# Kernel optimization log

Measured on AMD Instinct MI355X. Metric: run time of the kernel, lower is better.

## Reference

```python
import jax, jax.numpy as jnp
import numpy as np

N_FEATURES = 256
N_LAYERS = 256  # MZI layers; 2*N_LAYERS PSBS sublayers
BATCH = 1024


def _make_indexAB(nF):
    A = np.array([[2 * k, 2 * k + 1] for k in range(nF // 2)], np.int32)
    B = [[2 * k + 1, 2 * k + 2] for k in range((nF - 1) // 2)]
    while len(B) < nF // 2:
        B.append([-1, -1])  # padding sentinel, masked out
    return A, np.array(B, np.int32)


def _make_index(nF, nLayers):
    A, B = _make_indexAB(nF)
    blocks = ([A] * 2 + [B] * 2) * (nLayers // 2)
    if nLayers % 2 == 1:
        blocks += [A] * 2
    return np.stack(blocks).astype(np.int32)  # [2*nLayers, nF//2, 2]


def setup_inputs() -> dict:
    key = jax.random.key(0)
    k1, k2, k3 = jax.random.split(key, 3)
    nSub = 2 * N_LAYERS
    nAng = N_FEATURES // 2
    index = jnp.asarray(_make_index(N_FEATURES, N_LAYERS))
    return {
        "x_real": jax.random.normal(k1, (BATCH, N_FEATURES), jnp.float32),
        "x_imag": jax.random.normal(k2, (BATCH, N_FEATURES), jnp.float32),
        "params": jax.random.normal(k3, (nSub, nAng), jnp.float32),  # torch.randn init
        "ps_params": jnp.zeros((N_FEATURES,), jnp.float32),  # ModulePS zeros init
        "index": index,
        "split": jnp.zeros((nSub, nAng), jnp.float32),  # buffer, default zeros
        "atten": jnp.ones((nSub, N_FEATURES), jnp.float32),  # buffer, default ones
    }


def _psbs_mesh(x, params, i_safe, j_safe, valid, split, atten):
    # x: [B, F] complex64. Each sublayer: phase e^{i theta} on top port, then
    # beamsplitter [[cos a, i sin a],[i sin a, cos a]] with a = pi/4 + split,
    # then per-feature diagonal attenuation.
    def step(x, xs):
        theta, isf, jsf, vld, sp, at = xs
        xu = x[:, isf]  # [B, A]
        xv = x[:, jsf]
        u = xu * jnp.exp(1j * theta)[None, :]
        ang = jnp.float32(np.pi / 4) + sp
        t = jnp.cos(ang)
        r = jnp.sin(ang)
        yu = t * u + 1j * r * xv
        yv = 1j * r * u + t * xv
        zero = jnp.zeros((), x.dtype)
        # scatter deltas; invalid (padded) pairs add 0 so duplicate dummy index 0 is safe
        x = x.at[:, isf].add(jnp.where(vld, yu - xu, zero))
        x = x.at[:, jsf].add(jnp.where(vld, yv - xv, zero))
        return x * at[None, :], None

    x, _ = jax.lax.scan(step, x, (params, i_safe, j_safe, valid, split, atten))
    return x


def reference(x_real, x_imag, params, ps_params, index, split, atten):
    x = (x_real + 1j * x_imag).astype(jnp.complex64)
    i_idx = index[:, :, 0]
    j_idx = index[:, :, 1]
    valid = i_idx >= 0
    i_safe = jnp.where(valid, i_idx, 0)
    j_safe = jnp.where(valid, j_idx, 0)
    x = _psbs_mesh(x, params, i_safe, j_safe, valid, split, atten)
    # final diagonal phase shift (ModulePS)
    return x * jnp.exp(1j * ps_params)[None, :]
```

## Files before the change

### kernel.cpp

```cpp
#include <hip/hip_runtime.h>
#include <math.h>

#define NF   256
#define NSUB 512
#define NB   1024
#define BLOBF 768
#define WS_FLOATS (NSUB * BLOBF + NF * 2)
#define PI4 0.78539816339744830962f

__device__ __forceinline__ bool looks_zero(const void* p) {
  const unsigned* u = (const unsigned*)p;
  return (u[1] | u[25] | u[111]) == 0u;
}
__device__ __forceinline__ bool looks_ones(const void* p) {
  const unsigned* u = (const unsigned*)p;
  return u[1] == 0x3F800000u && u[3] == 0x3F800000u && u[257] == 0x3F800000u;
}

__global__ __launch_bounds__(256) void precompute_kernel(
    const void* __restrict__ pp0, const void* __restrict__ pp1,
    const void* __restrict__ pi0, const void* __restrict__ pi1,
    const float* __restrict__ psp, float* __restrict__ ws) {
  const float* params = looks_zero(pp0) ? (const float*)pp1 : (const float*)pp0;
  const float* split  = looks_zero(pp0) ? (const float*)pp0 : (const float*)pp1;
  const float* atten  = looks_ones(pi0) ? (const float*)pi0 : (const float*)pi1;
  const int s = blockIdx.x;
  const int t = threadIdx.x;
  if (s == NSUB) {
    float sn, cs;
    sincosf(psp[t], &sn, &cs);
    ((float2*)(ws + (size_t)NSUB * BLOBF))[t] = make_float2(cs, sn);
    return;
  }
  float* blob = ws + (size_t)s * BLOBF;
  if (t < 128) {
    float sn, cs, rr, tt;
    sincosf(params[s * 128 + t], &sn, &cs);
    sincosf(PI4 + split[s * 128 + t], &rr, &tt);
    *(float4*)(blob + (t >> 1) * 12 + (t & 1) * 4) = make_float4(cs, sn, tt, rr);
  } else if (t < 192) {
    const int l = t - 128;
    *(float4*)(blob + l * 12 + 8) = *(const float4*)(atten + (size_t)s * NF + 4 * l);
  }
}

struct Coef { float4 a, b, c; };

__device__ __forceinline__ Coef loadCoef(const char* p) {
  Coef k;
  k.a = *(const float4*)(p);
  k.b = *(const float4*)(p + 16);
  k.c = *(const float4*)(p + 32);
  return k;
}

__device__ __forceinline__ void mzi(float& ur, float& ui, float& vr, float& vi,
                                    const float4 k) {
  const float c = k.x, s = k.y, t = k.z, r = k.w;
  const float pr  = c * ur - s * ui;
  const float pi_ = s * ur + c * ui;
  const float nur = t * pr  - r * vi;
  const float nui = t * pi_ + r * vr;
  const float nvr = t * vr - r * pi_;
  const float nvi = t * vi + r * pr;
  ur = nur; ui = nui; vr = nvr; vi = nvi;
}

#define STATE float& x0r, float& x0i, float& x1r, float& x1i, \
              float& x2r, float& x2i, float& x3r, float& x3i

__device__ __forceinline__ void layerA(const Coef k, STATE) {
  mzi(x0r, x0i, x1r, x1i, k.a);
  mzi(x2r, x2i, x3r, x3i, k.b);
  x0r *= k.c.x; x0i *= k.c.x; x1r *= k.c.y; x1i *= k.c.y;
  x2r *= k.c.z; x2i *= k.c.z; x3r *= k.c.w; x3i *= k.c.w;
}

__device__ __forceinline__ void layerB(const Coef k, const int lane, STATE) {
  mzi(x1r, x1i, x2r, x2i, k.a);
  const float nvr = __shfl_down(x0r, 1);
  const float nvi = __shfl_down(x0i, 1);
  const float c = k.b.x, s = k.b.y, t = k.b.z, r = k.b.w;
  const float pr  = c * x3r - s * x3i;
  const float pi_ = s * x3r + c * x3i;
  const float yur = t * pr  - r * nvi;
  const float yui = t * pi_ + r * nvr;
  const float yvr = t * nvr - r * pi_;
  const float yvi = t * nvi + r * pr;
  const float svr = __shfl_up(yvr, 1);
  const float svi = __shfl_up(yvi, 1);
  if (lane < 63) { x3r = yur; x3i = yui; }
  if (lane > 0)  { x0r = svr; x0i = svi; }
  x0r *= k.c.x; x0i *= k.c.x; x1r *= k.c.y; x1i *= k.c.y;
  x2r *= k.c.z; x2i *= k.c.z; x3r *= k.c.w; x3i *= k.c.w;
}

__device__ __forceinline__ Coef makeCoefRaw(const float* __restrict__ params,
                                            const float* __restrict__ split,
                                            const float* __restrict__ atten,
                                            int s, int lane) {
  Coef k;
  const float2 th = *(const float2*)(params + (size_t)s * 128 + 2 * lane);
  const float2 sp = *(const float2*)(split + (size_t)s * 128 + 2 * lane);
  k.c = *(const float4*)(atten + (size_t)s * NF + 4 * lane);
  float sn, cs, rr, tt;
  __sincosf(th.x, &sn, &cs);
  __sincosf(PI4 + sp.x, &rr, &tt);
  k.a = make_float4(cs, sn, tt, rr);
  __sincosf(th.y, &sn, &cs);
  __sincosf(PI4 + sp.y, &rr, &tt);
  k.b = make_float4(cs, sn, tt, rr);
  return k;
}

#define PASS x0r, x0i, x1r, x1i, x2r, x2i, x3r, x3i

template <bool USE_WS>
__global__ __launch_bounds__(256) void mesh_kernel(
    const float* __restrict__ xr_in, const float* __restrict__ xi_in,
    const float* __restrict__ ws,
    const void* __restrict__ pp0, const void* __restrict__ pp1,
    const void* __restrict__ pi0, const void* __restrict__ pi1,
    const float* __restrict__ psp,
    float* __restrict__ out) {
  const int lane = threadIdx.x & 63;
  const int wv   = threadIdx.x >> 6;
  const int row  = blockIdx.x * 4 + wv;

  const float4 r4 = ((const float4*)(xr_in + (size_t)row * NF))[lane];
  const float4 i4 = ((const float4*)(xi_in + (size_t)row * NF))[lane];
  float x0r = r4.x, x1r = r4.y, x2r = r4.z, x3r = r4.w;
  float x0i = i4.x, x1i = i4.y, x2i = i4.z, x3i = i4.w;

  if (USE_WS) {
    const char* cp = (const char*)ws + lane * 48;
    Coef k0 = loadCoef(cp);
    Coef k1 = loadCoef(cp + 3072);
    Coef k2 = loadCoef(cp + 2 * 3072);
    Coef k3 = loadCoef(cp + 3 * 3072);
#pragma unroll 1
    for (int s = 0; s < NSUB; s += 4) {
      const char* np = cp + ((s + 4 < NSUB) ? 4 * 3072 : 0);
      Coef n0 = loadCoef(np);
      Coef n1 = loadCoef(np + 3072);
      Coef n2 = loadCoef(np + 2 * 3072);
      Coef n3 = loadCoef(np + 3 * 3072);
      layerA(k0, PASS);
      layerA(k1, PASS);
      layerB(k2, lane, PASS);
      layerB(k3, lane, PASS);
      k0 = n0; k1 = n1; k2 = n2; k3 = n3; cp = np;
    }
  } else {
    const float* params = looks_zero(pp0) ? (const float*)pp1 : (const float*)pp0;
    const float* split  = looks_zero(pp0) ? (const float*)pp0 : (const float*)pp1;
    const float* atten  = looks_ones(pi0) ? (const float*)pi0 : (const float*)pi1;
#pragma unroll 1
    for (int s = 0; s < NSUB; s += 4) {
      Coef k0 = makeCoefRaw(params, split, atten, s, lane);
      layerA(k0, PASS);
      Coef k1 = makeCoefRaw(params, split, atten, s + 1, lane);
      layerA(k1, PASS);
      Coef k2 = makeCoefRaw(params, split, atten, s + 2, lane);
      layerB(k2, lane, PASS);
      Coef k3 = makeCoefRaw(params, split, atten, s + 3, lane);
      layerB(k3, lane, PASS);
    }
  }

  float c0, s0, c1, s1, c2, s2, c3, s3;
  if (USE_WS) {
    const float2* psc = (const float2*)(ws + (size_t)NSUB * BLOBF);
    const float2 p0 = psc[4 * lane + 0];
    const float2 p1 = psc[4 * lane + 1];
    const float2 p2 = psc[4 * lane + 2];
    const float2 p3 = psc[4 * lane + 3];
    c0 = p0.x; s0 = p0.y; c1 = p1.x; s1 = p1.y;
    c2 = p2.x; s2 = p2.y; c3 = p3.x; s3 = p3.y;
  } else {
    sincosf(psp[4 * lane + 0], &s0, &c0);
    sincosf(psp[4 * lane + 1], &s1, &c1);
    sincosf(psp[4 * lane + 2], &s2, &c2);
    sincosf(psp[4 * lane + 3], &s3, &c3);
  }
  const float o0r = x0r * c0 - x0i * s0, o0i = x0r * s0 + x0i * c0;
  const float o1r = x1r * c1 - x1i * s1, o1i = x1r * s1 + x1i * c1;
  const float o2r = x2r * c2 - x2i * s2, o2i = x2r * s2 + x2i * c2;
  const float o3r = x3r * c3 - x3i * s3, o3i = x3r * s3 + x3i * c3;

  float4* op = (float4*)out;
  const size_t base = (size_t)row * 64 + lane;
  op[base] = make_float4(o0r, o1r, o2r, o3r);
  op[(size_t)NB * 64 + base] = make_float4(o0i, o1i, o2i, o3i);
}

extern "C" void kernel_launch(void* const* d_in, const int* in_sizes, int n_in,
                              void* d_out, int out_size, void* d_ws, size_t ws_size,
                              hipStream_t stream) {
  const void* px[2] = { d_in[0], d_in[1] };
  const void* pp[2] = { d_in[2], d_in[5] };
  const void* pi2[2] = { d_in[4], d_in[6] };
  const void* pps = d_in[3];
  {
    const void* sx[2]; const void* sp[2]; const void* si[2];
    const void* s256 = nullptr;
    int nx = 0, npp = 0, ni = 0;
    for (int i = 0; i < n_in; ++i) {
      const int sz = in_sizes[i];
      if (sz == 262144 && nx < 2)      sx[nx++] = d_in[i];
      else if (sz == 65536 && npp < 2) sp[npp++] = d_in[i];
      else if (sz == 131072 && ni < 2) si[ni++] = d_in[i];
      else if (sz == 256)              s256 = d_in[i];
    }
    if (nx == 2)  { px[0] = sx[0];  px[1] = sx[1]; }
    if (npp == 2) { pp[0] = sp[0];  pp[1] = sp[1]; }
    if (ni == 2)  { pi2[0] = si[0]; pi2[1] = si[1]; }
    if (s256)     pps = s256;
  }
  float* out = (float*)d_out;

  const size_t need = (size_t)WS_FLOATS * sizeof(float);
  if (ws_size >= need) {
    float* ws = (float*)d_ws;
    precompute_kernel<<<NSUB + 1, 256, 0, stream>>>(pp[0], pp[1], pi2[0], pi2[1],
                                                    (const float*)pps, ws);
    mesh_kernel<true><<<NB / 4, 256, 0, stream>>>(
        (const float*)px[0], (const float*)px[1], ws,
        pp[0], pp[1], pi2[0], pi2[1], (const float*)pps, out);
  } else {
    mesh_kernel<false><<<NB / 4, 256, 0, stream>>>(
        (const float*)px[0], (const float*)px[1], nullptr,
        pp[0], pp[1], pi2[0], pi2[1], (const float*)pps, out);
  }
}
```

Baseline: 79.90 us.

## Fuse consecutive same-index PSBS sublayer pairs into precomputed 2x2 complex matrices

Consecutive sublayers share the same pairing pattern (AA, BB), so each pair of phase-shift, beamsplitter and attenuation steps is folded into one complex 2x2 matrix per port pair. A precompute kernel writes 256 combined layers, and attenuation on unpaired boundary ports is folded into the matrices and the final phase table. The mesh kernel then does half as many sequential steps, with one shuffle pair per type-B layer, and re-indexes registers to handle the shifted B pairing. The cost is more coefficient data per step (32 vs 24 floats per lane) and more FLOPs per combined step.

```diff
diff --git a/kernel.cpp b/kernel.cpp
--- a/kernel.cpp
+++ b/kernel.cpp
@@ -1,11 +1,12 @@
 #include <hip/hip_runtime.h>
 #include <math.h>
 
-#define NF   256
-#define NSUB 512
-#define NB   1024
-#define BLOBF 768
-#define WS_FLOATS (NSUB * BLOBF + NF * 2)
+#define NF    256
+#define NSUB  512
+#define NB    1024
+#define NCOMB 256
+#define LAYER_F 1024
+#define WS_FLOATS2 (NCOMB * LAYER_F + 2 * NF)
 #define PI4 0.78539816339744830962f
 
 __device__ __forceinline__ bool looks_zero(const void* p) {
@@ -17,41 +18,141 @@
   return u[1] == 0x3F800000u && u[3] == 0x3F800000u && u[257] == 0x3F800000u;
 }
 
-__global__ __launch_bounds__(256) void precompute_kernel(
+__device__ __forceinline__ float2 cmul(float2 a, float2 b) {
+  return make_float2(a.x * b.x - a.y * b.y, a.x * b.y + a.y * b.x);
+}
+__device__ __forceinline__ float2 cadd(float2 a, float2 b) {
+  return make_float2(a.x + b.x, a.y + b.y);
+}
+__device__ __forceinline__ float2 csc(float2 a, float s) {
+  return make_float2(a.x * s, a.y * s);
+}
+
+__global__ __launch_bounds__(128) void precompute2_kernel(
     const void* __restrict__ pp0, const void* __restrict__ pp1,
     const void* __restrict__ pi0, const void* __restrict__ pi1,
     const float* __restrict__ psp, float* __restrict__ ws) {
   const float* params = looks_zero(pp0) ? (const float*)pp1 : (const float*)pp0;
   const float* split  = looks_zero(pp0) ? (const float*)pp0 : (const float*)pp1;
   const float* atten  = looks_ones(pi0) ? (const float*)pi0 : (const float*)pi1;
-  const int s = blockIdx.x;
-  const int t = threadIdx.x;
-  if (s == NSUB) {
-    float sn, cs;
-    sincosf(psp[t], &sn, &cs);
-    ((float2*)(ws + (size_t)NSUB * BLOBF))[t] = make_float2(cs, sn);
+  const int L = blockIdx.x;
+  const int k = threadIdx.x;
+
+  if (L == NCOMB) {
+#pragma unroll
+    for (int h = 0; h < 2; ++h) {
+      const int f = k + h * 128;
+      float sn, cs;
+      sincosf(psp[f], &sn, &cs);
+      if (f == 0) {
+        const float f0s = atten[510 * 256] * atten[511 * 256];
+        cs *= f0s; sn *= f0s;
+      }
+      ((float2*)(ws + (size_t)NCOMB * LAYER_F))[f] = make_float2(cs, sn);
+    }
     return;
   }
-  float* blob = ws + (size_t)s * BLOBF;
-  if (t < 128) {
-    float sn, cs, rr, tt;
-    sincosf(params[s * 128 + t], &sn, &cs);
-    sincosf(PI4 + split[s * 128 + t], &rr, &tt);
-    *(float4*)(blob + (t >> 1) * 12 + (t & 1) * 4) = make_float4(cs, sn, tt, rr);
-  } else if (t < 192) {
-    const int l = t - 128;
-    *(float4*)(blob + l * 12 + 8) = *(const float4*)(atten + (size_t)s * NF + 4 * l);
-  }
-}
-
-struct Coef { float4 a, b, c; };
-
-__device__ __forceinline__ Coef loadCoef(const char* p) {
-  Coef k;
-  k.a = *(const float4*)(p);
-  k.b = *(const float4*)(p + 16);
-  k.c = *(const float4*)(p + 32);
-  return k;
+
+  const int s1 = 2 * L, s2 = s1 + 1;
+  const bool typeB = (L & 1);
+  float2 C00, C01, C10, C11;
+  if (typeB && k == 127) {
+    const float a = atten[(size_t)s1 * NF + 255] * atten[(size_t)s2 * NF + 255];
+    C00 = make_float2(a, 0.f); C01 = make_float2(0.f, 0.f);
+    C10 = make_float2(0.f, 0.f); C11 = make_float2(0.f, 0.f);
+  } else {
+    const int i = typeB ? 2 * k + 1 : 2 * k;
+    const int j = i + 1;
+    float c1, s1v, t1, r1, c2, s2v, t2, r2;
+    sincosf(params[(size_t)s1 * 128 + k], &s1v, &c1);
+    sincosf(PI4 + split[(size_t)s1 * 128 + k], &r1, &t1);
+    sincosf(params[(size_t)s2 * 128 + k], &s2v, &c2);
+    sincosf(PI4 + split[(size_t)s2 * 128 + k], &r2, &t2);
+    const float a1i = atten[(size_t)s1 * NF + i], a1j = atten[(size_t)s1 * NF + j];
+    const float a2i = atten[(size_t)s2 * NF + i], a2j = atten[(size_t)s2 * NF + j];
+    const float2 Q00 = csc(make_float2(t1 * c1, t1 * s1v), a1i);
+    const float2 Q01 = csc(make_float2(0.f, r1), a1i);
+    const float2 Q10 = csc(make_float2(-r1 * s1v, r1 * c1), a1j);
+    const float2 Q11 = csc(make_float2(t1, 0.f), a1j);
+    const float2 P00 = csc(make_float2(t2 * c2, t2 * s2v), a2i);
+    const float2 P01 = csc(make_float2(0.f, r2), a2i);
+    const float2 P10 = csc(make_float2(-r2 * s2v, r2 * c2), a2j);
+    const float2 P11 = csc(make_float2(t2, 0.f), a2j);
+    C00 = cadd(cmul(P00, Q00), cmul(P01, Q10));
+    C01 = cadd(cmul(P00, Q01), cmul(P01, Q11));
+    C10 = cadd(cmul(P10, Q00), cmul(P11, Q10));
+    C11 = cadd(cmul(P10, Q01), cmul(P11, Q11));
+  }
+  if (!typeB && k == 0 && L > 0) {
+    const float f0s = atten[(size_t)(s1 - 2) * NF] * atten[(size_t)(s1 - 1) * NF];
+    C00 = csc(C00, f0s);
+    C10 = csc(C10, f0s);
+  }
+  float4* o = (float4*)(ws + (size_t)L * LAYER_F + (k >> 1) * 16 + (k & 1) * 8);
+  o[0] = make_float4(C00.x, C00.y, C01.x, C01.y);
+  o[1] = make_float4(C10.x, C10.y, C11.x, C11.y);
+}
+
+__device__ __forceinline__ void ap22(float& ur, float& ui, float& vr, float& vi,
+                                     const float4 m0, const float4 m1) {
+  const float nur = m0.x * ur - m0.y * ui + m0.z * vr - m0.w * vi;
+  const float nui = m0.x * ui + m0.y * ur + m0.z * vi + m0.w * vr;
+  const float nvr = m1.x * ur - m1.y * ui + m1.z * vr - m1.w * vi;
+  const float nvi = m1.x * ui + m1.y * ur + m1.z * vi + m1.w * vr;
+  ur = nur; ui = nui; vr = nvr; vi = nvi;
+}
+
+__global__ __launch_bounds__(256) void mesh2_kernel(
+    const float* __restrict__ xr_in, const float* __restrict__ xi_in,
+    const float* __restrict__ ws, float* __restrict__ out) {
+  const int lane = threadIdx.x & 63;
+  const int wv   = threadIdx.x >> 6;
+  const int row  = blockIdx.x * 4 + wv;
+
+  const float4 r4 = ((const float4*)(xr_in + (size_t)row * NF))[lane];
+  const float4 i4 = ((const float4*)(xi_in + (size_t)row * NF))[lane];
+  float x0r = r4.x, x1r = r4.y, x2r = r4.z, x3r = r4.w;
+  float x0i = i4.x, x1i = i4.y, x2i = i4.z, x3i = i4.w;
+
+  const float4* p = (const float4*)ws + lane * 4;
+  float4 A0 = p[0], A1 = p[1], A2 = p[2], A3 = p[3];
+  float4 B0 = p[256], B1 = p[257], B2 = p[258], B3 = p[259];
+#pragma unroll 1
+  for (int t = 0; t < 128; ++t) {
+    const float4* np = p + ((t < 127) ? 512 : 0);
+    const float4 nA0 = np[0], nA1 = np[1], nA2 = np[2], nA3 = np[3];
+    const float4 nB0 = np[256], nB1 = np[257], nB2 = np[258], nB3 = np[259];
+    ap22(x0r, x0i, x1r, x1i, A0, A1);
+    ap22(x2r, x2i, x3r, x3i, A2, A3);
+    const float s0r = x0r, s0i = x0i;
+    const float d3r = __shfl_down(x0r, 1), d3i = __shfl_down(x0i, 1);
+    x0r = x1r; x0i = x1i; x1r = x2r; x1i = x2i; x2r = x3r; x2i = x3i;
+    x3r = d3r; x3i = d3i;
+    ap22(x0r, x0i, x1r, x1i, B0, B1);
+    ap22(x2r, x2i, x3r, x3i, B2, B3);
+    const float u0r = __shfl_up(x3r, 1), u0i = __shfl_up(x3i, 1);
+    x3r = x2r; x3i = x2i; x2r = x1r; x2i = x1i; x1r = x0r; x1i = x0i;
+    x0r = lane ? u0r : s0r;
+    x0i = lane ? u0i : s0i;
+    A0 = nA0; A1 = nA1; A2 = nA2; A3 = nA3;
+    B0 = nB0; B1 = nB1; B2 = nB2; B3 = nB3;
+    p = np;
+  }
+
+  const float2* psc = (const float2*)(ws + (size_t)NCOMB * LAYER_F);
+  const float2 p0 = psc[4 * lane + 0];
+  const float2 p1 = psc[4 * lane + 1];
+  const float2 p2 = psc[4 * lane + 2];
+  const float2 p3 = psc[4 * lane + 3];
+  const float o0r = x0r * p0.x - x0i * p0.y, o0i = x0r * p0.y + x0i * p0.x;
+  const float o1r = x1r * p1.x - x1i * p1.y, o1i = x1r * p1.y + x1i * p1.x;
+  const float o2r = x2r * p2.x - x2i * p2.y, o2i = x2r * p2.y + x2i * p2.x;
+  const float o3r = x3r * p3.x - x3i * p3.y, o3i = x3r * p3.y + x3i * p3.x;
+
+  float4* op = (float4*)out;
+  const size_t base = (size_t)row * 64 + lane;
+  op[base] = make_float4(o0r, o1r, o2r, o3r);
+  op[(size_t)NB * 64 + base] = make_float4(o0i, o1i, o2i, o3i);
 }
 
 __device__ __forceinline__ void mzi(float& ur, float& ui, float& vr, float& vi,
@@ -65,17 +166,32 @@
   const float nvi = t * vi + r * pr;
   ur = nur; ui = nui; vr = nvr; vi = nvi;
 }
-
+struct Coef { float4 a, b, c; };
+__device__ __forceinline__ Coef makeCoefRaw(const float* __restrict__ params,
+                                            const float* __restrict__ split,
+                                            const float* __restrict__ atten,
+                                            int s, int lane) {
+  Coef k;
+  const float2 th = *(const float2*)(params + (size_t)s * 128 + 2 * lane);
+  const float2 sp = *(const float2*)(split + (size_t)s * 128 + 2 * lane);
+  k.c = *(const float4*)(atten + (size_t)s * NF + 4 * lane);
+  float sn, cs, rr, tt;
+  __sincosf(th.x, &sn, &cs);
+  __sincosf(PI4 + sp.x, &rr, &tt);
+  k.a = make_float4(cs, sn, tt, rr);
+  __sincosf(th.y, &sn, &cs);
+  __sincosf(PI4 + sp.y, &rr, &tt);
+  k.b = make_float4(cs, sn, tt, rr);
+  return k;
+}
 #define STATE float& x0r, float& x0i, float& x1r, float& x1i, \
               float& x2r, float& x2i, float& x3r, float& x3i
-
 __device__ __forceinline__ void layerA(const Coef k, STATE) {
   mzi(x0r, x0i, x1r, x1i, k.a);
   mzi(x2r, x2i, x3r, x3i, k.b);
   x0r *= k.c.x; x0i *= k.c.x; x1r *= k.c.y; x1i *= k.c.y;
   x2r *= k.c.z; x2i *= k.c.z; x3r *= k.c.w; x3i *= k.c.w;
 }
-
 __device__ __forceinline__ void layerB(const Coef k, const int lane, STATE) {
   mzi(x1r, x1i, x2r, x2i, k.a);
   const float nvr = __shfl_down(x0r, 1);
@@ -94,100 +210,42 @@
   x0r *= k.c.x; x0i *= k.c.x; x1r *= k.c.y; x1i *= k.c.y;
   x2r *= k.c.z; x2i *= k.c.z; x3r *= k.c.w; x3i *= k.c.w;
 }
-
-__device__ __forceinline__ Coef makeCoefRaw(const float* __restrict__ params,
-                                            const float* __restrict__ split,
-                                            const float* __restrict__ atten,
-                                            int s, int lane) {
-  Coef k;
-  const float2 th = *(const float2*)(params + (size_t)s * 128 + 2 * lane);
-  const float2 sp = *(const float2*)(split + (size_t)s * 128 + 2 * lane);
-  k.c = *(const float4*)(atten + (size_t)s * NF + 4 * lane);
-  float sn, cs, rr, tt;
-  __sincosf(th.x, &sn, &cs);
-  __sincosf(PI4 + sp.x, &rr, &tt);
-  k.a = make_float4(cs, sn, tt, rr);
-  __sincosf(th.y, &sn, &cs);
-  __sincosf(PI4 + sp.y, &rr, &tt);
-  k.b = make_float4(cs, sn, tt, rr);
-  return k;
-}
-
 #define PASS x0r, x0i, x1r, x1i, x2r, x2i, x3r, x3i
-
-template <bool USE_WS>
-__global__ __launch_bounds__(256) void mesh_kernel(
+__global__ __launch_bounds__(256) void mesh_raw_kernel(
     const float* __restrict__ xr_in, const float* __restrict__ xi_in,
-    const float* __restrict__ ws,
     const void* __restrict__ pp0, const void* __restrict__ pp1,
     const void* __restrict__ pi0, const void* __restrict__ pi1,
-    const float* __restrict__ psp,
-    float* __restrict__ out) {
+    const float* __restrict__ psp, float* __restrict__ out) {
   const int lane = threadIdx.x & 63;
   const int wv   = threadIdx.x >> 6;
   const int row  = blockIdx.x * 4 + wv;
-
   const float4 r4 = ((const float4*)(xr_in + (size_t)row * NF))[lane];
   const float4 i4 = ((const float4*)(xi_in + (size_t)row * NF))[lane];
   float x0r = r4.x, x1r = r4.y, x2r = r4.z, x3r = r4.w;
   float x0i = i4.x, x1i = i4.y, x2i = i4.z, x3i = i4.w;
-
-  if (USE_WS) {
-    const char* cp = (const char*)ws + lane * 48;
-    Coef k0 = loadCoef(cp);
-    Coef k1 = loadCoef(cp + 3072);
-    Coef k2 = loadCoef(cp + 2 * 3072);
-    Coef k3 = loadCoef(cp + 3 * 3072);
+  const float* params = looks_zero(pp0) ? (const float*)pp1 : (const float*)pp0;
+  const float* split  = looks_zero(pp0) ? (const float*)pp0 : (const float*)pp1;
+  const float* atten  = looks_ones(pi0) ? (const float*)pi0 : (const float*)pi1;
 #pragma unroll 1
-    for (int s = 0; s < NSUB; s += 4) {
-      const char* np = cp + ((s + 4 < NSUB) ? 4 * 3072 : 0);
-      Coef n0 = loadCoef(np);
-      Coef n1 = loadCoef(np + 3072);
-      Coef n2 = loadCoef(np + 2 * 3072);
-      Coef n3 = loadCoef(np + 3 * 3072);
-      layerA(k0, PASS);
-      layerA(k1, PASS);
-      layerB(k2, lane, PASS);
-      layerB(k3, lane, PASS);
-      k0 = n0; k1 = n1; k2 = n2; k3 = n3; cp = np;
-    }
-  } else {
-    const float* params = looks_zero(pp0) ? (const float*)pp1 : (const float*)pp0;
-    const float* split  = looks_zero(pp0) ? (const float*)pp0 : (const float*)pp1;
-    const float* atten  = looks_ones(pi0) ? (const float*)pi0 : (const float*)pi1;
-#pragma unroll 1
-    for (int s = 0; s < NSUB; s += 4) {
-      Coef k0 = makeCoefRaw(params, split, atten, s, lane);
-      layerA(k0, PASS);
-      Coef k1 = makeCoefRaw(params, split, atten, s + 1, lane);
-      layerA(k1, PASS);
-      Coef k2 = makeCoefRaw(params, split, atten, s + 2, lane);
-      layerB(k2, lane, PASS);
-      Coef k3 = makeCoefRaw(params, split, atten, s + 3, lane);
-      layerB(k3, lane, PASS);
-    }
-  }
-
+  for (int s = 0; s < NSUB; s += 4) {
+    Coef k0 = makeCoefRaw(params, split, atten, s, lane);
+    layerA(k0, PASS);
+    Coef k1 = makeCoefRaw(params, split, atten, s + 1, lane);
+    layerA(k1, PASS);
+    Coef k2 = makeCoefRaw(params, split, atten, s + 2, lane);
+    layerB(k2, lane, PASS);
+    Coef k3 = makeCoefRaw(params, split, atten, s + 3, lane);
+    layerB(k3, lane, PASS);
+  }
   float c0, s0, c1, s1, c2, s2, c3, s3;
-  if (USE_WS) {
-    const float2* psc = (const float2*)(ws + (size_t)NSUB * BLOBF);
-    const float2 p0 = psc[4 * lane + 0];
-    const float2 p1 = psc[4 * lane + 1];
-    const float2 p2 = psc[4 * lane + 2];
-    const float2 p3 = psc[4 * lane + 3];
-    c0 = p0.x; s0 = p0.y; c1 = p1.x; s1 = p1.y;
-    c2 = p2.x; s2 = p2.y; c3 = p3.x; s3 = p3.y;
-  } else {
-    sincosf(psp[4 * lane + 0], &s0, &c0);
-    sincosf(psp[4 * lane + 1], &s1, &c1);
-    sincosf(psp[4 * lane + 2], &s2, &c2);
-    sincosf(psp[4 * lane + 3], &s3, &c3);
-  }
+  sincosf(psp[4 * lane + 0], &s0, &c0);
+  sincosf(psp[4 * lane + 1], &s1, &c1);
+  sincosf(psp[4 * lane + 2], &s2, &c2);
+  sincosf(psp[4 * lane + 3], &s3, &c3);
   const float o0r = x0r * c0 - x0i * s0, o0i = x0r * s0 + x0i * c0;
   const float o1r = x1r * c1 - x1i * s1, o1i = x1r * s1 + x1i * c1;
   const float o2r = x2r * c2 - x2i * s2, o2i = x2r * s2 + x2i * c2;
   const float o3r = x3r * c3 - x3i * s3, o3i = x3r * s3 + x3i * c3;
-
   float4* op = (float4*)out;
   const size_t base = (size_t)row * 64 + lane;
   op[base] = make_float4(o0r, o1r, o2r, o3r);
@@ -219,17 +277,15 @@
   }
   float* out = (float*)d_out;
 
-  const size_t need = (size_t)WS_FLOATS * sizeof(float);
-  if (ws_size >= need) {
+  if (ws_size >= (size_t)WS_FLOATS2 * sizeof(float)) {
     float* ws = (float*)d_ws;
-    precompute_kernel<<<NSUB + 1, 256, 0, stream>>>(pp[0], pp[1], pi2[0], pi2[1],
-                                                    (const float*)pps, ws);
-    mesh_kernel<true><<<NB / 4, 256, 0, stream>>>(
-        (const float*)px[0], (const float*)px[1], ws,
+    precompute2_kernel<<<NCOMB + 1, 128, 0, stream>>>(
+        pp[0], pp[1], pi2[0], pi2[1], (const float*)pps, ws);
+    mesh2_kernel<<<NB / 4, 256, 0, stream>>>(
+        (const float*)px[0], (const float*)px[1], ws, out);
+  } else {
+    mesh_raw_kernel<<<NB / 4, 256, 0, stream>>>(
+        (const float*)px[0], (const float*)px[1],
         pp[0], pp[1], pi2[0], pi2[1], (const float*)pps, out);
-  } else {
-    mesh_kernel<false><<<NB / 4, 256, 0, stream>>>(
-        (const float*)px[0], (const float*)px[1], nullptr,
-        pp[0], pp[1], pi2[0], pi2[1], (const float*)pps, out);
-  }
-}
+  }
+}
```

New measurement: 72.50 us. 1.1x faster.
